# Kernel optimization log

Measured on AMD Instinct MI355X. Metric: run time of the kernel, lower is better.

## Reference

```python
import jax, jax.numpy as jnp
import numpy as np

N_CONTEXT = 256  # teacher-forced prefix length (n_context)
N_INPUTS = 2
HID = 16         # LSTM hidden_size
PROJ = 2         # LSTM proj_size


def setup_inputs() -> dict:
    key = jax.random.key(0)
    ks = jax.random.split(key, 6)
    B, T = 4096, 1024
    s = 1.0 / np.sqrt(HID)  # torch LSTM init range
    return {
        "u_train": jax.random.normal(ks[0], (B, T, N_INPUTS + PROJ), jnp.float32),
        "w_ih": jax.random.uniform(ks[1], (4 * HID, N_INPUTS), jnp.float32, -s, s),
        "w_hh": jax.random.uniform(ks[2], (4 * HID, PROJ), jnp.float32, -s, s),
        "b_ih": jax.random.uniform(ks[3], (4 * HID,), jnp.float32, -s, s),
        "b_hh": jax.random.uniform(ks[4], (4 * HID,), jnp.float32, -s, s),
        "w_hr": jax.random.uniform(ks[5], (PROJ, HID), jnp.float32, -s, s),
    }


def _cell(x, h, c, w_ih, w_hh, b, w_hr):
    # PyTorch LSTM gate order: i, f, g, o; projected output h = (o*tanh(c)) @ w_hr.T
    gates = x @ w_ih.T + h @ w_hh.T + b  # [B, 4*HID]
    i, f, g, o = jnp.split(gates, 4, axis=-1)
    c_new = jax.nn.sigmoid(f) * c + jax.nn.sigmoid(i) * jnp.tanh(g)
    h_new = (jax.nn.sigmoid(o) * jnp.tanh(c_new)) @ w_hr.T  # [B, PROJ]
    return h_new, c_new


def reference(u_train, w_ih, w_hh, b_ih, b_hh, w_hr):
    B = u_train.shape[0]
    u = u_train[..., :N_INPUTS]   # [B, T, 2] exogenous inputs
    y = u_train[..., N_INPUTS:]
    b = b_ih + b_hh

    xs_est = (jnp.swapaxes(u[:, :N_CONTEXT], 0, 1),  # [nstep, B, 2]
              jnp.swapaxes(y[:, :N_CONTEXT], 0, 1))
    c0 = jnp.zeros((B, HID), u_train.dtype)

    def est_step(c, xy):
        x_t, y_t = xy
        h_new, c_new = _cell(x_t, y_t, c, w_ih, w_hh, b, w_hr)
        return c_new, h_new

    cn, h_est = jax.lax.scan(est_step, c0, xs_est)  # h_est: [nstep, B, 2]
    hn = h_est[-1]

    # ---- predict_state: free-running LSTM from (hn, cn) ----
    def pred_step(carry, x_t):
        h, c = carry
        h_new, c_new = _cell(x_t, h, c, w_ih, w_hh, b, w_hr)
        return (h_new, c_new), h_new

    _, h_pred = jax.lax.scan(pred_step, (hn, cn), jnp.swapaxes(u[:, N_CONTEXT:], 0, 1))

    return jnp.concatenate([jnp.swapaxes(h_est, 0, 1), jnp.swapaxes(h_pred, 0, 1)], axis=1)
```

## Files before the change

### kernel.cpp

```cpp
#include <hip/hip_runtime.h>

#define N_CTX  256
#define T_LEN  1024
#define N_SEQ  4096
#define CHUNK  16
#define NCHUNK (T_LEN / CHUNK)
#define CTXCK  (N_CTX / CHUNK)

typedef float v2f __attribute__((ext_vector_type(2)));

__device__ __forceinline__ float fexp2(float x){ return __builtin_amdgcn_exp2f(x); }
__device__ __forceinline__ float frcp (float x){ return __builtin_amdgcn_rcpf(x); }
__device__ __forceinline__ v2f pk_fma(v2f a, v2f b, v2f c){ return __builtin_elementwise_fma(a, b, c); }

#define L1C 1.4426950408889634f
#define L2C 2.8853901631790583f
#define WCLAMP 100.0f

template<int CTRL>
__device__ __forceinline__ v2f dpp_add2(v2f x){
    int y0 = __builtin_amdgcn_mov_dpp(__float_as_int(x.x), CTRL, 0xf, 0xf, true);
    int y1 = __builtin_amdgcn_mov_dpp(__float_as_int(x.y), CTRL, 0xf, 0xf, true);
    v2f y = { __int_as_float(y0), __int_as_float(y1) };
    return x + y;
}
__device__ __forceinline__ v2f red16_2(v2f x){
    x = dpp_add2<0xB1>(x);
    x = dpp_add2<0x4E>(x);
    x = dpp_add2<0x124>(x);
    x = dpp_add2<0x128>(x);
    return x;
}

struct LaneW {
    v2f wi0_if, wi1_if, wi0_go, wi1_go;
    v2f wh0_if, wh1_if, wh0_go, wh1_go;
    v2f bs_if, bs_go;
    v2f whr;
};

struct ChunkX {
    v2f   xif[CHUNK];
    v2f   xgo[CHUNK];
    float y0[CHUNK], y1[CHUNK];
};

__device__ __forceinline__ void load_chunk(float4* b, const float4* __restrict__ up, int base){
#pragma unroll
    for (int i = 0; i < CHUNK; ++i) b[i] = up[base + i];
}

__device__ __forceinline__ void transform_chunk(ChunkX& X, const float4* raw, const LaneW& L){
#pragma unroll
    for (int i = 0; i < CHUNK; ++i) {
        const float4 x = raw[i];
        v2f xx = {x.x, x.x}, xy = {x.y, x.y};
        X.xif[i] = pk_fma(xy, L.wi1_if, pk_fma(xx, L.wi0_if, L.bs_if));
        X.xgo[i] = pk_fma(xy, L.wi1_go, pk_fma(xx, L.wi0_go, L.bs_go));
        X.y0[i]  = x.z;
        X.y1[i]  = x.w;
    }
}

template<bool TEACHER>
__device__ __forceinline__ void lstm_step(v2f xif, v2f xgo, float y0, float y1,
                                          const LaneW& L, float& c, v2f& rh)
{
    const float h0 = TEACHER ? y0 : rh.x;
    const float h1 = TEACHER ? y1 : rh.y;
    v2f hh0 = {h0, h0}, hh1 = {h1, h1};
    v2f gif = pk_fma(hh1, L.wh1_if, pk_fma(hh0, L.wh0_if, xif));
    v2f ggo = pk_fma(hh1, L.wh1_go, pk_fma(hh0, L.wh0_go, xgo));
    const float u  = fexp2(gif.x);
    const float ef = fexp2(gif.y);
    const float v  = fexp2(ggo.x);
    const float eo = fexp2(ggo.y);
    const float A   = (1.0f + u) * (v + 1.0f);
    const float B   = 1.0f + ef;
    const float t   = (v - 1.0f) * B;
    const float num = fmaf(c, A, t);
    c = num * frcp(A * B);
    const float w = fexp2(fminf(L2C * c, WCLAMP));
    const float s = (w - 1.0f) * frcp((1.0f + eo) * (w + 1.0f));
    v2f ss = {s, s};
    rh = red16_2(ss * L.whr);
}

template<bool TEACHER>
__device__ __forceinline__ void chain_chunk(const ChunkX& X, int baseT, const LaneW& L,
                                            float& c, v2f& rh,
                                            float4* __restrict__ opv, bool store_lane)
{
    float o[8];
#pragma unroll
    for (int i = 0; i < CHUNK; ++i) {
        lstm_step<TEACHER>(X.xif[i], X.xgo[i], X.y0[i], X.y1[i], L, c, rh);
        o[(i & 3) * 2]     = rh.x;
        o[(i & 3) * 2 + 1] = rh.y;
        if ((i & 3) == 3 && store_lane) {
            const int f4i = (baseT + i - 3) >> 1;
            opv[f4i]     = make_float4(o[0], o[1], o[2], o[3]);
            opv[f4i + 1] = make_float4(o[4], o[5], o[6], o[7]);
        }
    }
}

__global__ __launch_bounds__(256, 1) void openlstm_kernel(
    const float* __restrict__ u,
    const float* __restrict__ w_ih,
    const float* __restrict__ w_hh,
    const float* __restrict__ b_ih,
    const float* __restrict__ b_hh,
    const float* __restrict__ w_hr,
    float* __restrict__ out)
{
    const int tid = blockIdx.x * blockDim.x + threadIdx.x;
    const int seq = tid >> 4;
    const int j   = tid & 15;

    LaneW L;
    {
        const int ri = j, rf = 16 + j, rg = 32 + j, ro = 48 + j;
        const v2f sif = {-L1C, -L1C};
        const v2f sgo = { L2C, -L1C};
        L.wi0_if = sif * (v2f){w_ih[ri*2+0], w_ih[rf*2+0]};
        L.wi1_if = sif * (v2f){w_ih[ri*2+1], w_ih[rf*2+1]};
        L.wi0_go = sgo * (v2f){w_ih[rg*2+0], w_ih[ro*2+0]};
        L.wi1_go = sgo * (v2f){w_ih[rg*2+1], w_ih[ro*2+1]};
        L.wh0_if = sif * (v2f){w_hh[ri*2+0], w_hh[rf*2+0]};
        L.wh1_if = sif * (v2f){w_hh[ri*2+1], w_hh[rf*2+1]};
        L.wh0_go = sgo * (v2f){w_hh[rg*2+0], w_hh[ro*2+0]};
        L.wh1_go = sgo * (v2f){w_hh[rg*2+1], w_hh[ro*2+1]};
        L.bs_if  = sif * (v2f){b_ih[ri] + b_hh[ri], b_ih[rf] + b_hh[rf]};
        L.bs_go  = sgo * (v2f){b_ih[rg] + b_hh[rg], b_ih[ro] + b_hh[ro]};
        L.whr    = (v2f){w_hr[j], w_hr[16 + j]};
    }

    const float4* __restrict__ up = (const float4*)u + (size_t)seq * T_LEN;
    float4* __restrict__ opv = (float4*)((float2*)out + (size_t)seq * T_LEN);
    const bool sl = (j == 0);

    float c = 0.0f;
    v2f rh = {0.0f, 0.0f};
    float4 rawA[CHUNK], rawB[CHUNK];

    load_chunk(rawA, up, 0);
    load_chunk(rawB, up, CHUNK);

#pragma unroll 1
    for (int ck = 0; ck < NCHUNK; ck += 2) {
        {
            ChunkX XA;
            transform_chunk(XA, rawA, L);
            if (ck + 2 < NCHUNK) load_chunk(rawA, up, (ck + 2) * CHUNK);
            if (ck < CTXCK) chain_chunk<true >(XA, ck * CHUNK, L, c, rh, opv, sl);
            else            chain_chunk<false>(XA, ck * CHUNK, L, c, rh, opv, sl);
        }
        {
            ChunkX XB;
            transform_chunk(XB, rawB, L);
            if (ck + 3 < NCHUNK) load_chunk(rawB, up, (ck + 3) * CHUNK);
            if (ck + 1 < CTXCK) chain_chunk<true >(XB, (ck + 1) * CHUNK, L, c, rh, opv, sl);
            else                chain_chunk<false>(XB, (ck + 1) * CHUNK, L, c, rh, opv, sl);
        }
    }
}

extern "C" void kernel_launch(void* const* d_in, const int* in_sizes, int n_in,
                              void* d_out, int out_size, void* d_ws, size_t ws_size,
                              hipStream_t stream) {
    const float* u    = (const float*)d_in[0];
    const float* w_ih = (const float*)d_in[1];
    const float* w_hh = (const float*)d_in[2];
    const float* b_ih = (const float*)d_in[3];
    const float* b_hh = (const float*)d_in[4];
    const float* w_hr = (const float*)d_in[5];
    float* out = (float*)d_out;

    const int threads = 256;
    const int blocks  = (N_SEQ * 16) / threads;
    hipLaunchKernelGGL(openlstm_kernel, dim3(blocks), dim3(threads), 0, stream,
                       u, w_ih, w_hh, b_ih, b_hh, w_hr, out);
}
```

Baseline: 226.9 us.

## Distribute output stores across lanes and split teacher/free-run loops

Each of the 16 lanes of a sequence now captures the hidden output of one timestep per chunk and writes a single float2, so one coalesced store per chunk replaces lane-0 float4 stores every four steps. The main loop is split into a teacher-forced loop and a free-running loop, removing the per-chunk branching and the guarded prefetch conditions. In the free-running phase the y columns are no longer kept as chain inputs, which eases register pressure. The cost is a per-step select to capture the output, and the tail prefetches redundantly reload the last chunk.

```diff
diff --git a/kernel.cpp b/kernel.cpp
--- a/kernel.cpp
+++ b/kernel.cpp
@@ -50,6 +50,7 @@
     for (int i = 0; i < CHUNK; ++i) b[i] = up[base + i];
 }
 
+template<bool TEACHER>
 __device__ __forceinline__ void transform_chunk(ChunkX& X, const float4* raw, const LaneW& L){
 #pragma unroll
     for (int i = 0; i < CHUNK; ++i) {
@@ -57,8 +58,8 @@
         v2f xx = {x.x, x.x}, xy = {x.y, x.y};
         X.xif[i] = pk_fma(xy, L.wi1_if, pk_fma(xx, L.wi0_if, L.bs_if));
         X.xgo[i] = pk_fma(xy, L.wi1_go, pk_fma(xx, L.wi0_go, L.bs_go));
-        X.y0[i]  = x.z;
-        X.y1[i]  = x.w;
+        if (TEACHER) { X.y0[i] = x.z; X.y1[i] = x.w; }
+        else         { X.y0[i] = 0.f; X.y1[i] = 0.f; }
     }
 }
 
@@ -89,20 +90,16 @@
 template<bool TEACHER>
 __device__ __forceinline__ void chain_chunk(const ChunkX& X, int baseT, const LaneW& L,
                                             float& c, v2f& rh,
-                                            float4* __restrict__ opv, bool store_lane)
+                                            float2* __restrict__ op2, int j)
 {
-    float o[8];
+    v2f cap = rh;
 #pragma unroll
     for (int i = 0; i < CHUNK; ++i) {
         lstm_step<TEACHER>(X.xif[i], X.xgo[i], X.y0[i], X.y1[i], L, c, rh);
-        o[(i & 3) * 2]     = rh.x;
-        o[(i & 3) * 2 + 1] = rh.y;
-        if ((i & 3) == 3 && store_lane) {
-            const int f4i = (baseT + i - 3) >> 1;
-            opv[f4i]     = make_float4(o[0], o[1], o[2], o[3]);
-            opv[f4i + 1] = make_float4(o[4], o[5], o[6], o[7]);
-        }
+        cap = (j == i) ? rh : cap;
     }
+    float2 o; o.x = cap.x; o.y = cap.y;
+    op2[baseT + j] = o;
 }
 
 __global__ __launch_bounds__(256, 1) void openlstm_kernel(
@@ -137,8 +134,7 @@
     }
 
     const float4* __restrict__ up = (const float4*)u + (size_t)seq * T_LEN;
-    float4* __restrict__ opv = (float4*)((float2*)out + (size_t)seq * T_LEN);
-    const bool sl = (j == 0);
+    float2* __restrict__ op2 = (float2*)out + (size_t)seq * T_LEN;
 
     float c = 0.0f;
     v2f rh = {0.0f, 0.0f};
@@ -148,20 +144,36 @@
     load_chunk(rawB, up, CHUNK);
 
 #pragma unroll 1
-    for (int ck = 0; ck < NCHUNK; ck += 2) {
+    for (int ck = 0; ck < CTXCK; ck += 2) {
         {
             ChunkX XA;
-            transform_chunk(XA, rawA, L);
-            if (ck + 2 < NCHUNK) load_chunk(rawA, up, (ck + 2) * CHUNK);
-            if (ck < CTXCK) chain_chunk<true >(XA, ck * CHUNK, L, c, rh, opv, sl);
-            else            chain_chunk<false>(XA, ck * CHUNK, L, c, rh, opv, sl);
+            transform_chunk<true>(XA, rawA, L);
+            load_chunk(rawA, up, (ck + 2) * CHUNK);
+            chain_chunk<true>(XA, ck * CHUNK, L, c, rh, op2, j);
         }
         {
             ChunkX XB;
-            transform_chunk(XB, rawB, L);
-            if (ck + 3 < NCHUNK) load_chunk(rawB, up, (ck + 3) * CHUNK);
-            if (ck + 1 < CTXCK) chain_chunk<true >(XB, (ck + 1) * CHUNK, L, c, rh, opv, sl);
-            else                chain_chunk<false>(XB, (ck + 1) * CHUNK, L, c, rh, opv, sl);
+            transform_chunk<true>(XB, rawB, L);
+            load_chunk(rawB, up, (ck + 3) * CHUNK);
+            chain_chunk<true>(XB, (ck + 1) * CHUNK, L, c, rh, op2, j);
+        }
+    }
+
+#pragma unroll 1
+    for (int ck = CTXCK; ck < NCHUNK; ck += 2) {
+        const int lA = (ck + 2 < NCHUNK) ? (ck + 2) : (NCHUNK - 1);
+        const int lB = (ck + 3 < NCHUNK) ? (ck + 3) : (NCHUNK - 1);
+        {
+            ChunkX XA;
+            transform_chunk<false>(XA, rawA, L);
+            load_chunk(rawA, up, lA * CHUNK);
+            chain_chunk<false>(XA, ck * CHUNK, L, c, rh, op2, j);
+        }
+        {
+            ChunkX XB;
+            transform_chunk<false>(XB, rawB, L);
+            load_chunk(rawB, up, lB * CHUNK);
+            chain_chunk<false>(XB, (ck + 1) * CHUNK, L, c, rh, op2, j);
         }
     }
 }
```

Result: faster. 217.7 us (-4.1%).
